# Performance work log

Measured on AMD Instinct MI355X. Metric: run time of the kernel, lower is better.

Reference implementation:

```python
import jax, jax.numpy as jnp
import numpy as np

AREA = 8  # area_size


def setup_inputs() -> dict:
    key = jax.random.key(0)
    ks = jax.random.split(key, 8)
    b, c, h, w = 4, 256, 252, 252
    cr = c // 8  # reduction=8
    return {
        "x": jax.random.normal(ks[0], (b, c, h, w), jnp.float32),
        "Wq": jax.random.normal(ks[1], (cr, c), jnp.float32) * 0.05,
        "bq": jax.random.normal(ks[2], (cr,), jnp.float32) * 0.05,
        "Wk": jax.random.normal(ks[3], (cr, c), jnp.float32) * 0.05,
        "bk": jax.random.normal(ks[4], (cr,), jnp.float32) * 0.05,
        "Wv": jax.random.normal(ks[5], (c, c), jnp.float32) * 0.05,
        "bv": jax.random.normal(ks[6], (c,), jnp.float32) * 0.05,
        "gamma": jax.random.normal(ks[7], (1,), jnp.float32) * 0.1,
    }


def _conv1x1(x, W, bias):
    # x: [b,c,h,w], W: [o,c] -> [b,o,h,w]
    return jnp.einsum('bchw,oc->bohw', x, W) + bias[None, :, None, None]


def reference(x, Wq, bq, Wk, bk, Wv, bv, gamma):
    a = AREA
    b, c, h, w = x.shape
    ph = ((h - 1) // a + 1) * a
    pw = ((w - 1) // a + 1) * a
    xp = jnp.pad(x, ((0, 0), (0, 0), (0, ph - h), (0, pw - w)))

    q = _conv1x1(xp, Wq, bq)  # [b,cr,ph,pw]
    k = _conv1x1(xp, Wk, bk)  # [b,cr,ph,pw]
    v = _conv1x1(xp, Wv, bv)  # [b,c,ph,pw]

    nh, nw = ph // a, pw // a

    def window(t):
        # [b,C,ph,pw] -> [b*nh*nw, C, a*a]
        C = t.shape[1]
        t = t.reshape(b, C, nh, a, nw, a)
        t = t.transpose(0, 2, 4, 1, 3, 5)
        return t.reshape(b * nh * nw, C, a * a)

    qw, kw, vw = window(q), window(k), window(v)

    # attn[n,i,j] = sum_c q[n,c,i] * k[n,c,j]; softmax over j
    attn = jax.nn.softmax(jnp.einsum('nci,ncj->nij', qw, kw), axis=2)
    # out[n,c,i] = sum_j v[n,c,j] * attn[i,j]
    out = jnp.einsum('ncj,nij->nci', vw, attn)

    out = out.reshape(b, nh, nw, c, a, a)
    out = out.transpose(0, 3, 1, 4, 2, 5).reshape(b, c, ph, pw)
    out = out[:, :, :h, :w]
    return gamma * out + x
```

## Files before the change

kernel.cpp:

```cpp
#include <hip/hip_runtime.h>


#define HH 252
#define WW 252
#define CC 256
#define HW (HH * WW)

typedef __attribute__((ext_vector_type(8))) short bf8;
typedef __attribute__((ext_vector_type(4))) float f32x4;

__device__ __forceinline__ short f2bf(float f) {
    union { float f; unsigned u; } v; v.f = f;
    unsigned u = v.u;
    unsigned r = (u + 0x7fffu + ((u >> 16) & 1u)) >> 16;
    return (short)r;
}

__device__ __forceinline__ unsigned pk2(float a, float b) {
    return (unsigned)(unsigned short)f2bf(a) |
           ((unsigned)(unsigned short)f2bf(b) << 16);
}

__device__ __forceinline__ int xaddr(int p, int c) {
    int slot = (c >> 3) ^ ((p & 7) ^ ((p >> 3) & 7));
    return p * 256 + (slot << 3) + (c & 7);
}
__device__ __forceinline__ int vaddr(int c, int p) {
    int slot = ((p >> 3) ^ (c & 7)) & 7;
    return c * 64 + (slot << 3) + (p & 7);
}
__device__ __forceinline__ int qaddr(int p, int cr) {
    int slot = ((cr >> 3) ^ (p & 3)) & 3;
    return p * 32 + (slot << 3) + (cr & 7);
}
__device__ __forceinline__ int paddr(int i, int j) {
    int slot = ((j >> 3) ^ (i & 7)) & 7;
    return i * 64 + (slot << 3) + (j & 7);
}

__global__ __launch_bounds__(256) void prep_weights(
        const float* __restrict__ Wq, const float* __restrict__ Wk,
        const float* __restrict__ Wv, short* __restrict__ wf) {
    int t = blockIdx.x * 256 + threadIdx.x;
    if (t >= 81920) return;
    const float* W; int off, base;
    if (t < 8192)       { W = Wq; off = t;         base = 0; }
    else if (t < 16384) { W = Wk; off = t - 8192;  base = 8192; }
    else                { W = Wv; off = t - 16384; base = 16384; }
    int j = off & 7, l = (off >> 3) & 63, tile = off >> 9;
    int kt = tile & 7, mt = tile >> 3;
    int m = mt * 16 + (l & 15);
    int k = kt * 32 + ((l >> 4) * 8) + j;
    wf[base + off] = f2bf(W[m * 256 + k]);
}

__global__ __launch_bounds__(256, 4) void area_attn(
        const float* __restrict__ x, const short* __restrict__ wf,
        const float* __restrict__ bq, const float* __restrict__ bk,
        const float* __restrict__ bv, const float* __restrict__ gamma,
        float* __restrict__ out) {
    __shared__ short xs[16384];
    __shared__ short qk[4096];

    const int tid  = threadIdx.x;
    const int lane = tid & 63, wv = tid >> 6;
    const int l15  = lane & 15, quad = lane >> 4;

    const int bid  = blockIdx.x;
    const int xcd  = bid & 7;
    const int jb   = bid >> 3;
    const int nx   = jb & 31;
    const int grow = (jb >> 5) * 8 + xcd;
    const int bimg = grow >> 5;
    const int ny   = grow & 31;
    const int hb = ny * 8, wb = nx * 8;
    const float* xb = x   + (size_t)bimg * CC * HW;
    float*       ob = out + (size_t)bimg * CC * HW;

    const f32x4 zero4 = {0.f, 0.f, 0.f, 0.f};

    {
        int s = tid & 15, cg = tid >> 4;
        int h = hb + (s >> 1), w0 = wb + (s & 1) * 4;
        bool inb = (h < HH) && (w0 < WW);
        const float* src = xb + (size_t)h * WW + w0;
        int p0 = s * 4;
        #pragma unroll
        for (int it = 0; it < 4; ++it) {
            int c0 = it * 64 + cg * 4;
            float4 f[4];
            #pragma unroll
            for (int k = 0; k < 4; ++k) {
                if (inb) f[k] = *reinterpret_cast<const float4*>(src + (size_t)(c0 + k) * HW);
                else     f[k] = make_float4(0.f, 0.f, 0.f, 0.f);
            }
            #pragma unroll
            for (int i = 0; i < 4; ++i) {
                uint2 w2;
                w2.x = pk2(((const float*)&f[0])[i], ((const float*)&f[1])[i]);
                w2.y = pk2(((const float*)&f[2])[i], ((const float*)&f[3])[i]);
                *reinterpret_cast<uint2*>(&xs[xaddr(p0 + i, c0)]) = w2;
            }
        }
    }
    __syncthreads();

    {
        const bool isK = (wv >> 1) != 0;
        const int mt = wv & 1;
        const short* WFqk = wf + (isK ? 8192 : 0);
        f32x4 qacc[4];
        #pragma unroll
        for (int nt = 0; nt < 4; ++nt) qacc[nt] = zero4;
        #pragma unroll
        for (int kt = 0; kt < 8; ++kt) {
            bf8 aw = *reinterpret_cast<const bf8*>(
                WFqk + ((mt * 8 + kt) * 64 + lane) * 8);
            #pragma unroll
            for (int nt = 0; nt < 4; ++nt) {
                bf8 b = *reinterpret_cast<const bf8*>(
                    &xs[xaddr(nt * 16 + l15, kt * 32 + quad * 8)]);
                qacc[nt] = __builtin_amdgcn_mfma_f32_16x16x32_bf16(
                    aw, b, qacc[nt], 0, 0, 0);
            }
        }
        int cb = mt * 16 + quad * 4;
        const float* bias = isK ? bk : bq;
        float bi0 = bias[cb + 0], bi1 = bias[cb + 1];
        float bi2 = bias[cb + 2], bi3 = bias[cb + 3];
        short* dst = isK ? (qk + 2048) : qk;
        #pragma unroll
        for (int nt = 0; nt < 4; ++nt) {
            int pos = nt * 16 + l15;
            uint2 w2;
            w2.x = pk2(qacc[nt][0] + bi0, qacc[nt][1] + bi1);
            w2.y = pk2(qacc[nt][2] + bi2, qacc[nt][3] + bi3);
            *reinterpret_cast<uint2*>(&dst[qaddr(pos, cb)]) = w2;
        }
    }

    f32x4 vacc[4][4];
    #pragma unroll
    for (int t = 0; t < 4; ++t)
        #pragma unroll
        for (int ni = 0; ni < 4; ++ni) vacc[t][ni] = zero4;
    {
        #pragma unroll
        for (int kt = 0; kt < 8; ++kt) {
            bf8 xfr[4];
            #pragma unroll
            for (int t = 0; t < 4; ++t)
                xfr[t] = *reinterpret_cast<const bf8*>(
                    &xs[xaddr(t * 16 + l15, kt * 32 + quad * 8)]);
            #pragma unroll
            for (int ni = 0; ni < 4; ++ni) {
                bf8 bw = *reinterpret_cast<const bf8*>(
                    wf + 16384 + (((wv * 4 + ni) * 8 + kt) * 64 + lane) * 8);
                #pragma unroll
                for (int t = 0; t < 4; ++t)
                    vacc[t][ni] = __builtin_amdgcn_mfma_f32_16x16x32_bf16(
                        xfr[t], bw, vacc[t][ni], 0, 0, 0);
            }
        }
    }
    __syncthreads();

    #pragma unroll
    for (int ni = 0; ni < 4; ++ni) {
        int c = wv * 64 + ni * 16 + l15;
        float bvc = bv[c];
        #pragma unroll
        for (int t = 0; t < 4; ++t) {
            int p = t * 16 + quad * 4;
            uint2 w2;
            w2.x = pk2(vacc[t][ni][0] + bvc, vacc[t][ni][1] + bvc);
            w2.y = pk2(vacc[t][ni][2] + bvc, vacc[t][ni][3] + bvc);
            *reinterpret_cast<uint2*>(&xs[vaddr(c, p)]) = w2;
        }
    }
    bf8 aq = *reinterpret_cast<const bf8*>(&qk[qaddr(wv * 16 + l15, quad * 8)]);
    bf8 kb8[4];
    #pragma unroll
    for (int nt = 0; nt < 4; ++nt)
        kb8[nt] = *reinterpret_cast<const bf8*>(
            &qk[2048 + qaddr(nt * 16 + l15, quad * 8)]);
    __syncthreads();

    {
        f32x4 sacc[4];
        #pragma unroll
        for (int nt = 0; nt < 4; ++nt)
            sacc[nt] = __builtin_amdgcn_mfma_f32_16x16x32_bf16(
                aq, kb8[nt], zero4, 0, 0, 0);
        #pragma unroll
        for (int r = 0; r < 4; ++r) {
            float mx = fmaxf(fmaxf(sacc[0][r], sacc[1][r]),
                             fmaxf(sacc[2][r], sacc[3][r]));
            for (int m = 1; m < 16; m <<= 1) mx = fmaxf(mx, __shfl_xor(mx, m, 64));
            float e0 = __expf(sacc[0][r] - mx);
            float e1 = __expf(sacc[1][r] - mx);
            float e2 = __expf(sacc[2][r] - mx);
            float e3 = __expf(sacc[3][r] - mx);
            float sum = e0 + e1 + e2 + e3;
            for (int m = 1; m < 16; m <<= 1) sum += __shfl_xor(sum, m, 64);
            float inv = 1.f / sum;
            int i = wv * 16 + quad * 4 + r;
            qk[paddr(i,  0 + l15)] = f2bf(e0 * inv);
            qk[paddr(i, 16 + l15)] = f2bf(e1 * inv);
            qk[paddr(i, 32 + l15)] = f2bf(e2 * inv);
            qk[paddr(i, 48 + l15)] = f2bf(e3 * inv);
        }
    }
    __syncthreads();

    f32x4 oacc[4][4];
    #pragma unroll
    for (int mi = 0; mi < 4; ++mi)
        #pragma unroll
        for (int nt = 0; nt < 4; ++nt) oacc[mi][nt] = zero4;
    #pragma unroll
    for (int kt = 0; kt < 2; ++kt) {
        bf8 av[4], bp[4];
        #pragma unroll
        for (int mi = 0; mi < 4; ++mi)
            av[mi] = *reinterpret_cast<const bf8*>(
                &xs[vaddr((wv * 4 + mi) * 16 + l15, kt * 32 + quad * 8)]);
        #pragma unroll
        for (int nt = 0; nt < 4; ++nt)
            bp[nt] = *reinterpret_cast<const bf8*>(
                &qk[paddr(nt * 16 + l15, kt * 32 + quad * 8)]);
        #pragma unroll
        for (int nt = 0; nt < 4; ++nt)
            #pragma unroll
            for (int mi = 0; mi < 4; ++mi)
                oacc[mi][nt] = __builtin_amdgcn_mfma_f32_16x16x32_bf16(
                    av[mi], bp[nt], oacc[mi][nt], 0, 0, 0);
    }

    float g = gamma[0];
    #pragma unroll
    for (int nt = 0; nt < 4; ++nt) {
        int pos = nt * 16 + l15;
        int h = hb + (pos >> 3), w = wb + (pos & 7);
        if (h < HH && w < WW) {
            size_t idx = (size_t)h * WW + w;
            #pragma unroll
            for (int mi = 0; mi < 4; ++mi) {
                int c0 = (wv * 4 + mi) * 16 + quad * 4;
                #pragma unroll
                for (int r = 0; r < 4; ++r) {
                    size_t o = (size_t)(c0 + r) * HW + idx;
                    ob[o] = g * oacc[mi][nt][r] + xb[o];
                }
            }
        }
    }
}

extern "C" void kernel_launch(void* const* d_in, const int* in_sizes, int n_in,
                              void* d_out, int out_size, void* d_ws, size_t ws_size,
                              hipStream_t stream) {
    const float* x  = (const float*)d_in[0];
    const float* Wq = (const float*)d_in[1];
    const float* bq = (const float*)d_in[2];
    const float* Wk = (const float*)d_in[3];
    const float* bk = (const float*)d_in[4];
    const float* Wv = (const float*)d_in[5];
    const float* bv = (const float*)d_in[6];
    const float* gm = (const float*)d_in[7];
    short* wf = (short*)d_ws;

    prep_weights<<<320, 256, 0, stream>>>(Wq, Wk, Wv, wf);
    area_attn<<<4096, 256, 0, stream>>>(x, wf, bq, bk, bv, gm, (float*)d_out);
}
```

Baseline: 643.6 us.

## Process two adjacent windows per block and stage output through LDS for vector stores

```diff
diff --git a/kernel.cpp b/kernel.cpp
--- a/kernel.cpp
+++ b/kernel.cpp
@@ -36,6 +36,9 @@
 __device__ __forceinline__ int paddr(int i, int j) {
     int slot = ((j >> 3) ^ (i & 7)) & 7;
     return i * 64 + (slot << 3) + (j & 7);
+}
+__device__ __forceinline__ int saddr(int c, int P) {
+    return c * 128 + (P ^ ((c & 4) << 2));
 }
 
 __global__ __launch_bounds__(256) void prep_weights(
@@ -54,37 +57,44 @@
     wf[base + off] = f2bf(W[m * 256 + k]);
 }
 
-__global__ __launch_bounds__(256, 4) void area_attn(
+__global__ __launch_bounds__(512, 4) void area_attn(
         const float* __restrict__ x, const short* __restrict__ wf,
         const float* __restrict__ bq, const float* __restrict__ bk,
         const float* __restrict__ bv, const float* __restrict__ gamma,
         float* __restrict__ out) {
-    __shared__ short xs[16384];
-    __shared__ short qk[4096];
+    __shared__ __align__(16) short xs[32768];
+    __shared__ __align__(16) short qk[8192];
 
     const int tid  = threadIdx.x;
     const int lane = tid & 63, wv = tid >> 6;
+    const int win  = wv >> 2, wvv = wv & 3;
     const int l15  = lane & 15, quad = lane >> 4;
 
     const int bid  = blockIdx.x;
     const int xcd  = bid & 7;
     const int jb   = bid >> 3;
-    const int nx   = jb & 31;
-    const int grow = (jb >> 5) * 8 + xcd;
+    const int px   = jb & 15;
+    const int grow = (jb >> 4) * 8 + xcd;
     const int bimg = grow >> 5;
     const int ny   = grow & 31;
-    const int hb = ny * 8, wb = nx * 8;
+    const int hb = ny * 8, wb = px * 16;
     const float* xb = x   + (size_t)bimg * CC * HW;
     float*       ob = out + (size_t)bimg * CC * HW;
 
+    short* xsw = xs + win * 16384;
+    short* qkw = qk + win * 4096;
+
     const f32x4 zero4 = {0.f, 0.f, 0.f, 0.f};
 
     {
-        int s = tid & 15, cg = tid >> 4;
-        int h = hb + (s >> 1), w0 = wb + (s & 1) * 4;
-        bool inb = (h < HH) && (w0 < WW);
-        const float* src = xb + (size_t)h * WW + w0;
-        int p0 = s * 4;
+        int s = tid & 31, cg = tid >> 5;
+        int hl = s >> 2, w4 = s & 3;
+        int wn = w4 >> 1;
+        int p0 = hl * 8 + (w4 & 1) * 4;
+        int hg = hb + hl, w0 = wb + w4 * 4;
+        bool inb = (hg < HH) && (w0 < WW);
+        const float* src = xb + (size_t)hg * WW + w0;
+        short* dst = xs + wn * 16384;
         #pragma unroll
         for (int it = 0; it < 4; ++it) {
             int c0 = it * 64 + cg * 4;
@@ -99,15 +109,15 @@
                 uint2 w2;
                 w2.x = pk2(((const float*)&f[0])[i], ((const float*)&f[1])[i]);
                 w2.y = pk2(((const float*)&f[2])[i], ((const float*)&f[3])[i]);
-                *reinterpret_cast<uint2*>(&xs[xaddr(p0 + i, c0)]) = w2;
+                *reinterpret_cast<uint2*>(&dst[xaddr(p0 + i, c0)]) = w2;
             }
         }
     }
     __syncthreads();
 
     {
-        const bool isK = (wv >> 1) != 0;
-        const int mt = wv & 1;
+        const bool isK = (wvv >> 1) != 0;
+        const int mt = wvv & 1;
         const short* WFqk = wf + (isK ? 8192 : 0);
         f32x4 qacc[4];
         #pragma unroll
@@ -119,7 +129,7 @@
             #pragma unroll
             for (int nt = 0; nt < 4; ++nt) {
                 bf8 b = *reinterpret_cast<const bf8*>(
-                    &xs[xaddr(nt * 16 + l15, kt * 32 + quad * 8)]);
+                    &xsw[xaddr(nt * 16 + l15, kt * 32 + quad * 8)]);
                 qacc[nt] = __builtin_amdgcn_mfma_f32_16x16x32_bf16(
                     aw, b, qacc[nt], 0, 0, 0);
             }
@@ -128,7 +138,7 @@
         const float* bias = isK ? bk : bq;
         float bi0 = bias[cb + 0], bi1 = bias[cb + 1];
         float bi2 = bias[cb + 2], bi3 = bias[cb + 3];
-        short* dst = isK ? (qk + 2048) : qk;
+        short* dst = isK ? (qkw + 2048) : qkw;
         #pragma unroll
         for (int nt = 0; nt < 4; ++nt) {
             int pos = nt * 16 + l15;
@@ -151,11 +161,11 @@
             #pragma unroll
             for (int t = 0; t < 4; ++t)
                 xfr[t] = *reinterpret_cast<const bf8*>(
-                    &xs[xaddr(t * 16 + l15, kt * 32 + quad * 8)]);
+                    &xsw[xaddr(t * 16 + l15, kt * 32 + quad * 8)]);
             #pragma unroll
             for (int ni = 0; ni < 4; ++ni) {
                 bf8 bw = *reinterpret_cast<const bf8*>(
-                    wf + 16384 + (((wv * 4 + ni) * 8 + kt) * 64 + lane) * 8);
+                    wf + 16384 + (((wvv * 4 + ni) * 8 + kt) * 64 + lane) * 8);
                 #pragma unroll
                 for (int t = 0; t < 4; ++t)
                     vacc[t][ni] = __builtin_amdgcn_mfma_f32_16x16x32_bf16(
@@ -167,7 +177,7 @@
 
     #pragma unroll
     for (int ni = 0; ni < 4; ++ni) {
-        int c = wv * 64 + ni * 16 + l15;
+        int c = wvv * 64 + ni * 16 + l15;
         float bvc = bv[c];
         #pragma unroll
         for (int t = 0; t < 4; ++t) {
@@ -175,15 +185,15 @@
             uint2 w2;
             w2.x = pk2(vacc[t][ni][0] + bvc, vacc[t][ni][1] + bvc);
             w2.y = pk2(vacc[t][ni][2] + bvc, vacc[t][ni][3] + bvc);
-            *reinterpret_cast<uint2*>(&xs[vaddr(c, p)]) = w2;
-        }
-    }
-    bf8 aq = *reinterpret_cast<const bf8*>(&qk[qaddr(wv * 16 + l15, quad * 8)]);
+            *reinterpret_cast<uint2*>(&xsw[vaddr(c, p)]) = w2;
+        }
+    }
+    bf8 aq = *reinterpret_cast<const bf8*>(&qkw[qaddr(wvv * 16 + l15, quad * 8)]);
     bf8 kb8[4];
     #pragma unroll
     for (int nt = 0; nt < 4; ++nt)
         kb8[nt] = *reinterpret_cast<const bf8*>(
-            &qk[2048 + qaddr(nt * 16 + l15, quad * 8)]);
+            &qkw[2048 + qaddr(nt * 16 + l15, quad * 8)]);
     __syncthreads();
 
     {
@@ -204,11 +214,11 @@
             float sum = e0 + e1 + e2 + e3;
             for (int m = 1; m < 16; m <<= 1) sum += __shfl_xor(sum, m, 64);
             float inv = 1.f / sum;
-            int i = wv * 16 + quad * 4 + r;
-            qk[paddr(i,  0 + l15)] = f2bf(e0 * inv);
-            qk[paddr(i, 16 + l15)] = f2bf(e1 * inv);
-            qk[paddr(i, 32 + l15)] = f2bf(e2 * inv);
-            qk[paddr(i, 48 + l15)] = f2bf(e3 * inv);
+            int i = wvv * 16 + quad * 4 + r;
+            qkw[paddr(i,  0 + l15)] = f2bf(e0 * inv);
+            qkw[paddr(i, 16 + l15)] = f2bf(e1 * inv);
+            qkw[paddr(i, 32 + l15)] = f2bf(e2 * inv);
+            qkw[paddr(i, 48 + l15)] = f2bf(e3 * inv);
         }
     }
     __syncthreads();
@@ -224,11 +234,11 @@
         #pragma unroll
         for (int mi = 0; mi < 4; ++mi)
             av[mi] = *reinterpret_cast<const bf8*>(
-                &xs[vaddr((wv * 4 + mi) * 16 + l15, kt * 32 + quad * 8)]);
+                &xsw[vaddr((wvv * 4 + mi) * 16 + l15, kt * 32 + quad * 8)]);
         #pragma unroll
         for (int nt = 0; nt < 4; ++nt)
             bp[nt] = *reinterpret_cast<const bf8*>(
-                &qk[paddr(nt * 16 + l15, kt * 32 + quad * 8)]);
+                &qkw[paddr(nt * 16 + l15, kt * 32 + quad * 8)]);
         #pragma unroll
         for (int nt = 0; nt < 4; ++nt)
             #pragma unroll
@@ -236,24 +246,46 @@
                 oacc[mi][nt] = __builtin_amdgcn_mfma_f32_16x16x32_bf16(
                     av[mi], bp[nt], oacc[mi][nt], 0, 0, 0);
     }
-
+    __syncthreads();
+
+    float* st = (float*)xs;
     float g = gamma[0];
     #pragma unroll
-    for (int nt = 0; nt < 4; ++nt) {
-        int pos = nt * 16 + l15;
-        int h = hb + (pos >> 3), w = wb + (pos & 7);
-        if (h < HH && w < WW) {
-            size_t idx = (size_t)h * WW + w;
+    for (int Hh = 0; Hh < 2; ++Hh) {
+        if ((wvv >> 1) == Hh) {
             #pragma unroll
             for (int mi = 0; mi < 4; ++mi) {
-                int c0 = (wv * 4 + mi) * 16 + quad * 4;
+                int cl = (wvv & 1) * 64 + mi * 16 + quad * 4;
                 #pragma unroll
-                for (int r = 0; r < 4; ++r) {
-                    size_t o = (size_t)(c0 + r) * HW + idx;
-                    ob[o] = g * oacc[mi][nt][r] + xb[o];
+                for (int nt = 0; nt < 4; ++nt) {
+                    int P = win * 64 + nt * 16 + l15;
+                    #pragma unroll
+                    for (int r = 0; r < 4; ++r)
+                        st[saddr(cl + r, P)] = oacc[mi][nt][r];
                 }
             }
         }
+        __syncthreads();
+        #pragma unroll
+        for (int i = 0; i < 8; ++i) {
+            int idx = i * 512 + tid;
+            int c = idx >> 5, p4 = idx & 31;
+            int P = p4 * 4;
+            int wn = P >> 6, pos = P & 63;
+            int hg = hb + (pos >> 3), wg = wb + wn * 8 + (pos & 7);
+            if (hg < HH && wg < WW) {
+                size_t o = (size_t)(Hh * 128 + c) * HW + (size_t)hg * WW + wg;
+                float4 xv = *reinterpret_cast<const float4*>(xb + o);
+                f32x4 sv = *reinterpret_cast<const f32x4*>(&st[saddr(c, P)]);
+                float4 ov;
+                ov.x = g * sv[0] + xv.x;
+                ov.y = g * sv[1] + xv.y;
+                ov.z = g * sv[2] + xv.z;
+                ov.w = g * sv[3] + xv.w;
+                *reinterpret_cast<float4*>(ob + o) = ov;
+            }
+        }
+        __syncthreads();
     }
 }
 
@@ -271,5 +303,5 @@
     short* wf = (short*)d_ws;
 
     prep_weights<<<320, 256, 0, stream>>>(Wq, Wk, Wv, wf);
-    area_attn<<<4096, 256, 0, stream>>>(x, wf, bq, bk, bv, gm, (float*)d_out);
-}
+    area_attn<<<2048, 512, 0, stream>>>(x, wf, bq, bk, bv, gm, (float*)d_out);
+}
```

Result: faster. 558.2 us (-13.3%).
